# Optimization experiments

Hardware: AMD Instinct MI355X
Metric: run time of the kernel (lower is better)

## Reference

```python
import jax, jax.numpy as jnp
import numpy as np

VV = 100000   # value vocab
VP = 100000   # path vocab
VT = 50257    # tag vocab
E = 128       # embedding size
B = 2048      # batch of functions
N = 10        # rep_size (contexts per function)


def setup_inputs() -> dict:
    key = jax.random.key(0)
    ks = jax.random.split(key, 10)
    return {
        "value1_idx": jax.random.randint(ks[0], (B, N), 0, VV),
        "path_idx": jax.random.randint(ks[1], (B, N), 0, VP),
        "value2_idx": jax.random.randint(ks[2], (B, N), 0, VV),
        "value_emb": jax.random.normal(ks[3], (VV, E), jnp.float32) * 0.02,
        "path_emb": jax.random.normal(ks[4], (VP, E), jnp.float32) * 0.02,
        "tag_emb": jax.random.normal(ks[5], (VT, E), jnp.float32) * 0.02,
        "W_fc": jax.random.normal(ks[6], (3 * E, E), jnp.float32) * 0.02,
        "b_fc": jnp.zeros((E,), jnp.float32),
        "w_att": jax.random.normal(ks[7], (E,), jnp.float32) * 0.02,
        "b_att": jnp.zeros((), jnp.float32),
    }


def reference(value1_idx, path_idx, value2_idx, value_emb, path_emb, tag_emb,
              W_fc, b_fc, w_att, b_att):
    # Per-context embedding gathers: [B, N, E]
    v1 = value_emb[value1_idx]
    p = path_emb[path_idx]
    v2 = value_emb[value2_idx]
    ctx = jnp.concatenate([v1, p, v2], axis=-1)          # [B, N, 3E]
    c_tilde = jnp.tanh(ctx @ W_fc + b_fc)                # [B, N, E]
    # Attention pooling over the N contexts
    att = jax.nn.softmax(c_tilde @ w_att + b_att, axis=1)  # [B, N]
    v = jnp.einsum('bne,bn->be', c_tilde, att)           # [B, E]
    # Softmax classifier over all tags
    logits = v @ tag_emb.T                               # [B, VT]
    q = jax.nn.softmax(logits, axis=-1)
    return q
```

## Files before the change

### kernel.cpp

```cpp
#include <hip/hip_runtime.h>
#include <hip/hip_bf16.h>
#include <math.h>

#define VTAG 50257
#define EDIM 128
#define NREP 10
#define BFUNC 2048
#define NSTRIP 786
#define NPAD (NSTRIP * 64)

typedef __bf16 bf16x8 __attribute__((ext_vector_type(8)));
typedef float f32x4 __attribute__((ext_vector_type(4)));

__device__ __forceinline__ unsigned short f2bf(float x) {
    unsigned u = __float_as_uint(x);
    unsigned r = (u + 0x7fffu + ((u >> 16) & 1u)) >> 16;
    return (unsigned short)r;
}

__global__ __launch_bounds__(128) void k1_attn(
    const int* __restrict__ v1i, const int* __restrict__ pti,
    const int* __restrict__ v2i,
    const float* __restrict__ vemb, const float* __restrict__ pemb,
    const float* __restrict__ Wfc, const float* __restrict__ bfc,
    const float* __restrict__ watt, const float* __restrict__ batt,
    unsigned short* __restrict__ vbf)
{
    const int b = blockIdx.x;
    const int e = threadIdx.x;
    __shared__ float ctx[NREP][3 * EDIM];
    __shared__ float red[2][NREP];

    #pragma unroll
    for (int j = 0; j < 30; ++j) {
        int i = j * 128 + e;
        int n = i / 384;
        int c = i - n * 384;
        float val;
        if (c < 128)      val = vemb[(size_t)v1i[b * NREP + n] * EDIM + c];
        else if (c < 256) val = pemb[(size_t)pti[b * NREP + n] * EDIM + (c - 128)];
        else              val = vemb[(size_t)v2i[b * NREP + n] * EDIM + (c - 256)];
        ctx[n][c] = val;
    }
    __syncthreads();

    float acc[NREP];
    #pragma unroll
    for (int n = 0; n < NREP; ++n) acc[n] = 0.f;

    for (int k = 0; k < 384; k += 4) {
        float w0 = Wfc[(k + 0) * EDIM + e];
        float w1 = Wfc[(k + 1) * EDIM + e];
        float w2 = Wfc[(k + 2) * EDIM + e];
        float w3 = Wfc[(k + 3) * EDIM + e];
        #pragma unroll
        for (int n = 0; n < NREP; ++n) {
            float4 c4 = *(const float4*)&ctx[n][k];
            acc[n] = fmaf(c4.x, w0, acc[n]);
            acc[n] = fmaf(c4.y, w1, acc[n]);
            acc[n] = fmaf(c4.z, w2, acc[n]);
            acc[n] = fmaf(c4.w, w3, acc[n]);
        }
    }

    const float bias = bfc[e];
    const float we = watt[e];
    float ct[NREP];
    #pragma unroll
    for (int n = 0; n < NREP; ++n) ct[n] = tanhf(acc[n] + bias);

    const int wv = e >> 6, ln = e & 63;
    #pragma unroll
    for (int n = 0; n < NREP; ++n) {
        float p = ct[n] * we;
        p += __shfl_xor(p, 32);
        p += __shfl_xor(p, 16);
        p += __shfl_xor(p, 8);
        p += __shfl_xor(p, 4);
        p += __shfl_xor(p, 2);
        p += __shfl_xor(p, 1);
        if (ln == 0) red[wv][n] = p;
    }
    __syncthreads();

    const float batt0 = batt[0];
    float al[NREP];
    float m = -1e30f;
    #pragma unroll
    for (int n = 0; n < NREP; ++n) {
        al[n] = red[0][n] + red[1][n] + batt0;
        m = fmaxf(m, al[n]);
    }
    float s = 0.f;
    #pragma unroll
    for (int n = 0; n < NREP; ++n) { al[n] = __expf(al[n] - m); s += al[n]; }
    const float inv = 1.f / s;

    float v = 0.f;
    #pragma unroll
    for (int n = 0; n < NREP; ++n) v = fmaf(al[n] * inv, ct[n], v);

    vbf[b * EDIM + e] = f2bf(v);
}

__global__ __launch_bounds__(256) void k_conv_tag(
    const float* __restrict__ tag, unsigned short* __restrict__ tbf)
{
    size_t i = ((size_t)blockIdx.x * 256 + threadIdx.x) * 4;
    if (i >= (size_t)NPAD * EDIM) return;
    float4 x = make_float4(0.f, 0.f, 0.f, 0.f);
    if (i < (size_t)VTAG * EDIM) x = *(const float4*)(tag + i);
    ushort4 o;
    o.x = f2bf(x.x); o.y = f2bf(x.y); o.z = f2bf(x.z); o.w = f2bf(x.w);
    *(ushort4*)(tbf + i) = o;
}

__global__ __launch_bounds__(256) void k2_logits(
    const unsigned short* __restrict__ vbf, const unsigned short* __restrict__ tbf,
    float* __restrict__ out, float* __restrict__ pmax, float* __restrict__ psum)
{
    const int wave = threadIdx.x >> 6;
    const int lane = threadIdx.x & 63;
    const int quad = lane >> 4;
    const int l16  = lane & 15;
    const int strip = blockIdx.y;
    const int n0 = strip * 64;
    const int rowbase = blockIdx.x * 128 + wave * 32;

    const bf16x8* tb8 = (const bf16x8*)tbf;
    const bf16x8* vb8 = (const bf16x8*)vbf;

    bf16x8 bfrag[4][4];
    #pragma unroll
    for (int nt = 0; nt < 4; ++nt) {
        int col = n0 + nt * 16 + l16;
        const bf16x8* p = tb8 + (size_t)col * 16 + quad;
        #pragma unroll
        for (int ks = 0; ks < 4; ++ks) bfrag[nt][ks] = p[ks * 4];
    }
    bf16x8 afrag[2][4];
    #pragma unroll
    for (int mt = 0; mt < 2; ++mt) {
        int row = rowbase + mt * 16 + l16;
        const bf16x8* p = vb8 + (size_t)row * 16 + quad;
        #pragma unroll
        for (int ks = 0; ks < 4; ++ks) afrag[mt][ks] = p[ks * 4];
    }

    f32x4 acc[2][4];
    #pragma unroll
    for (int mt = 0; mt < 2; ++mt)
        #pragma unroll
        for (int nt = 0; nt < 4; ++nt) acc[mt][nt] = (f32x4){0.f, 0.f, 0.f, 0.f};

    #pragma unroll
    for (int ks = 0; ks < 4; ++ks)
        #pragma unroll
        for (int mt = 0; mt < 2; ++mt)
            #pragma unroll
            for (int nt = 0; nt < 4; ++nt)
                acc[mt][nt] = __builtin_amdgcn_mfma_f32_16x16x32_bf16(
                    afrag[mt][ks], bfrag[nt][ks], acc[mt][nt], 0, 0, 0);

    #pragma unroll
    for (int mt = 0; mt < 2; ++mt) {
        #pragma unroll
        for (int r = 0; r < 4; ++r) {
            const int row = rowbase + mt * 16 + quad * 4 + r;
            float lm = -1e30f;
            #pragma unroll
            for (int nt = 0; nt < 4; ++nt) {
                int col = n0 + nt * 16 + l16;
                float x = acc[mt][nt][r];
                if (col < VTAG) lm = fmaxf(lm, x);
            }
            lm = fmaxf(lm, __shfl_xor(lm, 1));
            lm = fmaxf(lm, __shfl_xor(lm, 2));
            lm = fmaxf(lm, __shfl_xor(lm, 4));
            lm = fmaxf(lm, __shfl_xor(lm, 8));
            float ls = 0.f;
            #pragma unroll
            for (int nt = 0; nt < 4; ++nt) {
                int col = n0 + nt * 16 + l16;
                float x = acc[mt][nt][r];
                if (col < VTAG) {
                    ls += __expf(x - lm);
                    out[(size_t)row * VTAG + col] = x;
                }
            }
            ls += __shfl_xor(ls, 1);
            ls += __shfl_xor(ls, 2);
            ls += __shfl_xor(ls, 4);
            ls += __shfl_xor(ls, 8);
            if (l16 == 0) {
                pmax[(size_t)row * NSTRIP + strip] = lm;
                psum[(size_t)row * NSTRIP + strip] = ls;
            }
        }
    }
}

__global__ __launch_bounds__(256) void k3_reduce(
    const float* __restrict__ pmax, const float* __restrict__ psum,
    float* __restrict__ rowM, float* __restrict__ rowR)
{
    const int row = blockIdx.x * 4 + (threadIdx.x >> 6);
    const int ln = threadIdx.x & 63;
    const float* pm = pmax + (size_t)row * NSTRIP;
    const float* ps = psum + (size_t)row * NSTRIP;

    float m = -1e30f;
    for (int i = ln; i < NSTRIP; i += 64) m = fmaxf(m, pm[i]);
    m = fmaxf(m, __shfl_xor(m, 32));
    m = fmaxf(m, __shfl_xor(m, 16));
    m = fmaxf(m, __shfl_xor(m, 8));
    m = fmaxf(m, __shfl_xor(m, 4));
    m = fmaxf(m, __shfl_xor(m, 2));
    m = fmaxf(m, __shfl_xor(m, 1));

    float s = 0.f;
    for (int i = ln; i < NSTRIP; i += 64) s += ps[i] * __expf(pm[i] - m);
    s += __shfl_xor(s, 32);
    s += __shfl_xor(s, 16);
    s += __shfl_xor(s, 8);
    s += __shfl_xor(s, 4);
    s += __shfl_xor(s, 2);
    s += __shfl_xor(s, 1);

    if (ln == 0) { rowM[row] = m; rowR[row] = 1.f / s; }
}

__global__ __launch_bounds__(256) void k4_norm(
    float* __restrict__ out, const float* __restrict__ rowM,
    const float* __restrict__ rowR)
{
    unsigned i0 = (blockIdx.x * 256u + threadIdx.x) * 4u;
    const unsigned total = (unsigned)BFUNC * VTAG;
    if (i0 >= total) return;
    unsigned row = i0 / VTAG;
    unsigned c = i0 - row * VTAG;
    if (c + 4 <= VTAG) {
        float M = rowM[row], R = rowR[row];
        float4 x = *(float4*)(out + i0);
        x.x = __expf(x.x - M) * R;
        x.y = __expf(x.y - M) * R;
        x.z = __expf(x.z - M) * R;
        x.w = __expf(x.w - M) * R;
        *(float4*)(out + i0) = x;
    } else {
        #pragma unroll
        for (int j = 0; j < 4; ++j) {
            unsigned i = i0 + j;
            unsigned r2 = i / VTAG;
            out[i] = __expf(out[i] - rowM[r2]) * rowR[r2];
        }
    }
}

extern "C" void kernel_launch(void* const* d_in, const int* in_sizes, int n_in,
                              void* d_out, int out_size, void* d_ws, size_t ws_size,
                              hipStream_t stream)
{
    const int*   v1i  = (const int*)d_in[0];
    const int*   pti  = (const int*)d_in[1];
    const int*   v2i  = (const int*)d_in[2];
    const float* vemb = (const float*)d_in[3];
    const float* pemb = (const float*)d_in[4];
    const float* temb = (const float*)d_in[5];
    const float* Wfc  = (const float*)d_in[6];
    const float* bfc  = (const float*)d_in[7];
    const float* watt = (const float*)d_in[8];
    const float* batt = (const float*)d_in[9];
    float* out = (float*)d_out;

    char* ws = (char*)d_ws;
    const size_t vbf_off  = 0;
    const size_t tbf_off  = vbf_off + 524288;
    const size_t pmax_off = tbf_off + 12877824;
    const size_t psum_off = pmax_off + 6438912;
    const size_t rowm_off = psum_off + 6438912;
    const size_t rowr_off = rowm_off + 8192;

    unsigned short* vbf = (unsigned short*)(ws + vbf_off);
    unsigned short* tbf = (unsigned short*)(ws + tbf_off);
    float* pmax = (float*)(ws + pmax_off);
    float* psum = (float*)(ws + psum_off);
    float* rowM = (float*)(ws + rowm_off);
    float* rowR = (float*)(ws + rowr_off);

    hipLaunchKernelGGL(k1_attn, dim3(BFUNC), dim3(128), 0, stream,
                       v1i, pti, v2i, vemb, pemb, Wfc, bfc, watt, batt, vbf);
    hipLaunchKernelGGL(k_conv_tag, dim3((NPAD * EDIM / 4 + 255) / 256), dim3(256),
                       0, stream, temb, tbf);
    hipLaunchKernelGGL(k2_logits, dim3(BFUNC / 128, NSTRIP), dim3(256), 0, stream,
                       vbf, tbf, out, pmax, psum);
    hipLaunchKernelGGL(k3_reduce, dim3(BFUNC / 4), dim3(256), 0, stream,
                       pmax, psum, rowM, rowR);
    hipLaunchKernelGGL(k4_norm, dim3(((unsigned)BFUNC * VTAG / 4 + 255) / 256),
                       dim3(256), 0, stream, out, rowM, rowR);
}
```

Measured before the change: 812.7 us.

## Recompute logits in final pass instead of storing and renormalizing them

The logits kernel now emits only per-strip max and sum partials and no longer writes the full logits matrix. A new final kernel recomputes the bf16 MFMA logits tile and writes the normalized softmax directly using the per-row max and reciprocal sum. This removes one full write and one read-modify-write pass over the large output, in exchange for doing the small-K matmul twice.

```diff
diff --git a/kernel.cpp b/kernel.cpp
--- a/kernel.cpp
+++ b/kernel.cpp
@@ -115,9 +115,9 @@
     *(ushort4*)(tbf + i) = o;
 }
 
-__global__ __launch_bounds__(256) void k2_logits(
+__global__ __launch_bounds__(256) void k2_partial(
     const unsigned short* __restrict__ vbf, const unsigned short* __restrict__ tbf,
-    float* __restrict__ out, float* __restrict__ pmax, float* __restrict__ psum)
+    float* __restrict__ pmax, float* __restrict__ psum)
 {
     const int wave = threadIdx.x >> 6;
     const int lane = threadIdx.x & 63;
@@ -183,10 +183,7 @@
             for (int nt = 0; nt < 4; ++nt) {
                 int col = n0 + nt * 16 + l16;
                 float x = acc[mt][nt][r];
-                if (col < VTAG) {
-                    ls += __expf(x - lm);
-                    out[(size_t)row * VTAG + col] = x;
-                }
+                if (col < VTAG) ls += __expf(x - lm);
             }
             ls += __shfl_xor(ls, 1);
             ls += __shfl_xor(ls, 2);
@@ -230,29 +227,78 @@
     if (ln == 0) { rowM[row] = m; rowR[row] = 1.f / s; }
 }
 
-__global__ __launch_bounds__(256) void k4_norm(
-    float* __restrict__ out, const float* __restrict__ rowM,
-    const float* __restrict__ rowR)
-{
-    unsigned i0 = (blockIdx.x * 256u + threadIdx.x) * 4u;
-    const unsigned total = (unsigned)BFUNC * VTAG;
-    if (i0 >= total) return;
-    unsigned row = i0 / VTAG;
-    unsigned c = i0 - row * VTAG;
-    if (c + 4 <= VTAG) {
-        float M = rowM[row], R = rowR[row];
-        float4 x = *(float4*)(out + i0);
-        x.x = __expf(x.x - M) * R;
-        x.y = __expf(x.y - M) * R;
-        x.z = __expf(x.z - M) * R;
-        x.w = __expf(x.w - M) * R;
-        *(float4*)(out + i0) = x;
-    } else {
-        #pragma unroll
-        for (int j = 0; j < 4; ++j) {
-            unsigned i = i0 + j;
-            unsigned r2 = i / VTAG;
-            out[i] = __expf(out[i] - rowM[r2]) * rowR[r2];
+__global__ __launch_bounds__(256) void k4_write(
+    const unsigned short* __restrict__ vbf, const unsigned short* __restrict__ tbf,
+    const float* __restrict__ rowM, const float* __restrict__ rowR,
+    float* __restrict__ out)
+{
+    const int wave = threadIdx.x >> 6;
+    const int lane = threadIdx.x & 63;
+    const int quad = lane >> 4;
+    const int l16  = lane & 15;
+    const int strip = blockIdx.y;
+    const int n0 = strip * 64;
+    const int rowbase = blockIdx.x * 128 + wave * 32;
+
+    const bf16x8* tb8 = (const bf16x8*)tbf;
+    const bf16x8* vb8 = (const bf16x8*)vbf;
+
+    float Mv[2][4], Rv[2][4];
+    #pragma unroll
+    for (int mt = 0; mt < 2; ++mt)
+        #pragma unroll
+        for (int r = 0; r < 4; ++r) {
+            const int row = rowbase + mt * 16 + quad * 4 + r;
+            Mv[mt][r] = rowM[row];
+            Rv[mt][r] = rowR[row];
+        }
+
+    bf16x8 bfrag[4][4];
+    #pragma unroll
+    for (int nt = 0; nt < 4; ++nt) {
+        int col = n0 + nt * 16 + l16;
+        const bf16x8* p = tb8 + (size_t)col * 16 + quad;
+        #pragma unroll
+        for (int ks = 0; ks < 4; ++ks) bfrag[nt][ks] = p[ks * 4];
+    }
+    bf16x8 afrag[2][4];
+    #pragma unroll
+    for (int mt = 0; mt < 2; ++mt) {
+        int row = rowbase + mt * 16 + l16;
+        const bf16x8* p = vb8 + (size_t)row * 16 + quad;
+        #pragma unroll
+        for (int ks = 0; ks < 4; ++ks) afrag[mt][ks] = p[ks * 4];
+    }
+
+    f32x4 acc[2][4];
+    #pragma unroll
+    for (int mt = 0; mt < 2; ++mt)
+        #pragma unroll
+        for (int nt = 0; nt < 4; ++nt) acc[mt][nt] = (f32x4){0.f, 0.f, 0.f, 0.f};
+
+    #pragma unroll
+    for (int ks = 0; ks < 4; ++ks)
+        #pragma unroll
+        for (int mt = 0; mt < 2; ++mt)
+            #pragma unroll
+            for (int nt = 0; nt < 4; ++nt)
+                acc[mt][nt] = __builtin_amdgcn_mfma_f32_16x16x32_bf16(
+                    afrag[mt][ks], bfrag[nt][ks], acc[mt][nt], 0, 0, 0);
+
+    #pragma unroll
+    for (int mt = 0; mt < 2; ++mt) {
+        #pragma unroll
+        for (int r = 0; r < 4; ++r) {
+            const int row = rowbase + mt * 16 + quad * 4 + r;
+            const float M = Mv[mt][r];
+            const float R = Rv[mt][r];
+            #pragma unroll
+            for (int nt = 0; nt < 4; ++nt) {
+                int col = n0 + nt * 16 + l16;
+                if (col < VTAG)
+                    out[(size_t)row * VTAG + col] =
+                        __expf(acc[mt][nt][r] - M) * R;
+            }
         }
     }
 }
@@ -292,10 +338,10 @@
                        v1i, pti, v2i, vemb, pemb, Wfc, bfc, watt, batt, vbf);
     hipLaunchKernelGGL(k_conv_tag, dim3((NPAD * EDIM / 4 + 255) / 256), dim3(256),
                        0, stream, temb, tbf);
-    hipLaunchKernelGGL(k2_logits, dim3(BFUNC / 128, NSTRIP), dim3(256), 0, stream,
-                       vbf, tbf, out, pmax, psum);
+    hipLaunchKernelGGL(k2_partial, dim3(BFUNC / 128, NSTRIP), dim3(256), 0, stream,
+                       vbf, tbf, pmax, psum);
     hipLaunchKernelGGL(k3_reduce, dim3(BFUNC / 4), dim3(256), 0, stream,
                        pmax, psum, rowM, rowR);
-    hipLaunchKernelGGL(k4_norm, dim3(((unsigned)BFUNC * VTAG / 4 + 255) / 256),
-                       dim3(256), 0, stream, out, rowM, rowR);
-}
+    hipLaunchKernelGGL(k4_write, dim3(BFUNC / 128, NSTRIP), dim3(256), 0, stream,
+                       vbf, tbf, rowM, rowR, out);
+}
```

Result: slower. 833.6 us (+2.6%).
